# Optimization experiments

Hardware: AMD Instinct MI355X
Metric: run time of the kernel (lower is better)

Reference implementation:

```python
import jax, jax.numpy as jnp
import numpy as np

N_TOKENS = 32768
INPUT_DIM = 1024
HIDDEN_DIM = 256
NUM_EXPERTS = 64
TOP_K = 2


def setup_inputs() -> dict:
    key = jax.random.key(0)
    kx, k1, k2, kb1, kb2 = jax.random.split(key, 5)
    # torch nn.Linear init scale ~ U(-1/sqrt(fan_in), 1/sqrt(fan_in)); use small normals
    x = jax.random.normal(kx, (N_TOKENS, INPUT_DIM), dtype=jnp.float32)
    w1 = jax.random.normal(k1, (HIDDEN_DIM, INPUT_DIM), dtype=jnp.float32) / np.sqrt(INPUT_DIM)
    b1 = jax.random.normal(kb1, (HIDDEN_DIM,), dtype=jnp.float32) * 0.01
    w2 = jax.random.normal(k2, (NUM_EXPERTS, HIDDEN_DIM), dtype=jnp.float32) / np.sqrt(HIDDEN_DIM)
    b2 = jax.random.normal(kb2, (NUM_EXPERTS,), dtype=jnp.float32) * 0.01
    return {"x": x, "w1": w1, "b1": b1, "w2": w2, "b2": b2}


def reference(x, w1, b1, w2, b2):
    # logits = Linear -> ReLU -> Linear
    h = jax.nn.relu(jnp.einsum("nd,hd->nh", x, w1) + b1)       # [N, hidden]
    logits = jnp.einsum("nh,eh->ne", h, w2) + b2               # [N, experts]
    top_k_logits, top_k_indices = jax.lax.top_k(logits, TOP_K)  # [N, k]
    top_k_gates = jax.nn.softmax(top_k_logits, axis=-1)
    return top_k_indices, top_k_gates
```

## Files before the change

### kernel.cpp

```cpp
#include <hip/hip_runtime.h>
#include <math.h>

#define N_TOK 32768
#define IN_DIM 1024
#define HID 256
#define NE 64

__global__ __launch_bounds__(256, 2)
void gemm1_relu(const float* __restrict__ x, const float* __restrict__ w1,
                const float* __restrict__ b1, float* __restrict__ h)
{
    __shared__ float Xs[32][72];
    __shared__ float Ws[32][256];

    const int tid = threadIdx.x;
    const int t0  = blockIdx.x * 64;
    const int tg  = tid >> 5;
    const int hg  = tid & 31;

    float acc[8][8];
    #pragma unroll
    for (int i = 0; i < 8; ++i)
        #pragma unroll
        for (int j = 0; j < 8; ++j) acc[i][j] = 0.f;

    for (int k0 = 0; k0 < IN_DIM; k0 += 32) {
        #pragma unroll
        for (int r = 0; r < 2; ++r) {
            int slot = tid + 256 * r;
            int t  = slot >> 3;
            int kq = (slot & 7) * 4;
            float4 v = *(const float4*)(x + (size_t)(t0 + t) * IN_DIM + k0 + kq);
            Xs[kq + 0][t] = v.x; Xs[kq + 1][t] = v.y;
            Xs[kq + 2][t] = v.z; Xs[kq + 3][t] = v.w;
        }
        #pragma unroll
        for (int r = 0; r < 8; ++r) {
            int slot = tid + 256 * r;
            int hh = slot >> 3;
            int kq = (slot & 7) * 4;
            float4 v = *(const float4*)(w1 + (size_t)hh * IN_DIM + k0 + kq);
            Ws[kq + 0][hh] = v.x; Ws[kq + 1][hh] = v.y;
            Ws[kq + 2][hh] = v.z; Ws[kq + 3][hh] = v.w;
        }
        __syncthreads();

        #pragma unroll
        for (int k = 0; k < 32; ++k) {
            float xv[8], wv[8];
            *(float4*)&xv[0] = *(const float4*)&Xs[k][tg * 8];
            *(float4*)&xv[4] = *(const float4*)&Xs[k][tg * 8 + 4];
            *(float4*)&wv[0] = *(const float4*)&Ws[k][hg * 8];
            *(float4*)&wv[4] = *(const float4*)&Ws[k][hg * 8 + 4];
            #pragma unroll
            for (int i = 0; i < 8; ++i)
                #pragma unroll
                for (int j = 0; j < 8; ++j)
                    acc[i][j] = fmaf(xv[i], wv[j], acc[i][j]);
        }
        __syncthreads();
    }

    float4 bv0 = *(const float4*)(b1 + hg * 8);
    float4 bv1 = *(const float4*)(b1 + hg * 8 + 4);
    float bias[8] = {bv0.x, bv0.y, bv0.z, bv0.w, bv1.x, bv1.y, bv1.z, bv1.w};
    #pragma unroll
    for (int i = 0; i < 8; ++i) {
        int t = t0 + tg * 8 + i;
        float4 o0, o1;
        o0.x = fmaxf(acc[i][0] + bias[0], 0.f);
        o0.y = fmaxf(acc[i][1] + bias[1], 0.f);
        o0.z = fmaxf(acc[i][2] + bias[2], 0.f);
        o0.w = fmaxf(acc[i][3] + bias[3], 0.f);
        o1.x = fmaxf(acc[i][4] + bias[4], 0.f);
        o1.y = fmaxf(acc[i][5] + bias[5], 0.f);
        o1.z = fmaxf(acc[i][6] + bias[6], 0.f);
        o1.w = fmaxf(acc[i][7] + bias[7], 0.f);
        *(float4*)(h + (size_t)t * HID + hg * 8)     = o0;
        *(float4*)(h + (size_t)t * HID + hg * 8 + 4) = o1;
    }
}

__global__ __launch_bounds__(256, 2)
void gemm2_topk(const float* __restrict__ h, const float* __restrict__ w2,
                const float* __restrict__ b2, float* __restrict__ out)
{
    __shared__ float Hs[32][72];
    __shared__ float W2s[32][64];
    __shared__ float Ls[64][65];

    const int tid = threadIdx.x;
    const int t0  = blockIdx.x * 64;
    const int tg  = tid >> 4;
    const int eg  = tid & 15;

    float acc[4][4];
    #pragma unroll
    for (int i = 0; i < 4; ++i)
        #pragma unroll
        for (int j = 0; j < 4; ++j) acc[i][j] = 0.f;

    for (int k0 = 0; k0 < HID; k0 += 32) {
        #pragma unroll
        for (int r = 0; r < 2; ++r) {
            int slot = tid + 256 * r;
            int t  = slot >> 3;
            int kq = (slot & 7) * 4;
            float4 v = *(const float4*)(h + (size_t)(t0 + t) * HID + k0 + kq);
            Hs[kq + 0][t] = v.x; Hs[kq + 1][t] = v.y;
            Hs[kq + 2][t] = v.z; Hs[kq + 3][t] = v.w;
        }
        #pragma unroll
        for (int r = 0; r < 2; ++r) {
            int slot = tid + 256 * r;
            int e  = slot >> 3;
            int kq = (slot & 7) * 4;
            float4 v = *(const float4*)(w2 + (size_t)e * HID + k0 + kq);
            W2s[kq + 0][e] = v.x; W2s[kq + 1][e] = v.y;
            W2s[kq + 2][e] = v.z; W2s[kq + 3][e] = v.w;
        }
        __syncthreads();

        #pragma unroll
        for (int k = 0; k < 32; ++k) {
            float hv[4], wv[4];
            *(float4*)&hv[0] = *(const float4*)&Hs[k][tg * 4];
            *(float4*)&wv[0] = *(const float4*)&W2s[k][eg * 4];
            #pragma unroll
            for (int i = 0; i < 4; ++i)
                #pragma unroll
                for (int j = 0; j < 4; ++j)
                    acc[i][j] = fmaf(hv[i], wv[j], acc[i][j]);
        }
        __syncthreads();
    }

    float4 b2v = *(const float4*)(b2 + eg * 4);
    float bb[4] = {b2v.x, b2v.y, b2v.z, b2v.w};
    #pragma unroll
    for (int i = 0; i < 4; ++i)
        #pragma unroll
        for (int j = 0; j < 4; ++j)
            Ls[tg * 4 + i][eg * 4 + j] = acc[i][j] + bb[j];
    __syncthreads();

    if (tid < 64) {
        const int t = tid;
        float m1 = -INFINITY, m2 = -INFINITY;
        int i1 = 0, i2 = 0;
        #pragma unroll 8
        for (int e = 0; e < NE; ++e) {
            float v = Ls[t][e];
            if (v > m1) { m2 = m1; i2 = i1; m1 = v; i1 = e; }
            else if (v > m2) { m2 = v; i2 = e; }
        }
        float e2  = expf(m2 - m1);
        float inv = 1.f / (1.f + e2);
        float g1  = inv;
        float g2  = e2 * inv;
        int gt = t0 + t;
        out[(size_t)gt * 2 + 0] = (float)i1;
        out[(size_t)gt * 2 + 1] = (float)i2;
        out[(size_t)2 * N_TOK + (size_t)gt * 2 + 0] = g1;
        out[(size_t)2 * N_TOK + (size_t)gt * 2 + 1] = g2;
    }
}

extern "C" void kernel_launch(void* const* d_in, const int* in_sizes, int n_in,
                              void* d_out, int out_size, void* d_ws, size_t ws_size,
                              hipStream_t stream) {
    const float* x  = (const float*)d_in[0];
    const float* w1 = (const float*)d_in[1];
    const float* b1 = (const float*)d_in[2];
    const float* w2 = (const float*)d_in[3];
    const float* b2 = (const float*)d_in[4];
    float* out = (float*)d_out;
    float* h   = (float*)d_ws;

    gemm1_relu<<<N_TOK / 64, 256, 0, stream>>>(x, w1, b1, h);
    gemm2_topk<<<N_TOK / 64, 256, 0, stream>>>(h, w2, b2, out);
}
```

Before: 416.5 us.

## Register-prefetch next K tile, remap wave tiling and pad shared arrays

```diff
diff --git a/kernel.cpp b/kernel.cpp
--- a/kernel.cpp
+++ b/kernel.cpp
@@ -6,17 +6,28 @@
 #define HID 256
 #define NE 64
 
+#define PX 68
+#define PW 260
+#define PL 65
+
 __global__ __launch_bounds__(256, 2)
 void gemm1_relu(const float* __restrict__ x, const float* __restrict__ w1,
                 const float* __restrict__ b1, float* __restrict__ h)
 {
-    __shared__ float Xs[32][72];
-    __shared__ float Ws[32][256];
-
-    const int tid = threadIdx.x;
-    const int t0  = blockIdx.x * 64;
-    const int tg  = tid >> 5;
-    const int hg  = tid & 31;
+    __shared__ float Xs[32 * PX];
+    __shared__ float Ws[32 * PW];
+
+    const int tid  = threadIdx.x;
+    const int t0   = blockIdx.x * 64;
+    const int wave = tid >> 6;
+    const int lane = tid & 63;
+    const int tg   = lane >> 3;
+    const int hg   = lane & 7;
+    const int xoff = tg * 8;
+    const int woff = wave * 64 + hg * 8;
+
+    const int tx = tid >> 3;
+    const int kq = (tid & 7) * 4;
 
     float acc[8][8];
     #pragma unroll
@@ -24,49 +35,65 @@
         #pragma unroll
         for (int j = 0; j < 8; ++j) acc[i][j] = 0.f;
 
-    for (int k0 = 0; k0 < IN_DIM; k0 += 32) {
-        #pragma unroll
-        for (int r = 0; r < 2; ++r) {
-            int slot = tid + 256 * r;
-            int t  = slot >> 3;
-            int kq = (slot & 7) * 4;
-            float4 v = *(const float4*)(x + (size_t)(t0 + t) * IN_DIM + k0 + kq);
-            Xs[kq + 0][t] = v.x; Xs[kq + 1][t] = v.y;
-            Xs[kq + 2][t] = v.z; Xs[kq + 3][t] = v.w;
-        }
-        #pragma unroll
-        for (int r = 0; r < 8; ++r) {
-            int slot = tid + 256 * r;
-            int hh = slot >> 3;
-            int kq = (slot & 7) * 4;
-            float4 v = *(const float4*)(w1 + (size_t)hh * IN_DIM + k0 + kq);
-            Ws[kq + 0][hh] = v.x; Ws[kq + 1][hh] = v.y;
-            Ws[kq + 2][hh] = v.z; Ws[kq + 3][hh] = v.w;
-        }
-        __syncthreads();
+    float4 xr0, xr1, wr[8];
+    {
+        xr0 = *(const float4*)(x + (size_t)(t0 + tx) * IN_DIM + kq);
+        xr1 = *(const float4*)(x + (size_t)(t0 + tx + 32) * IN_DIM + kq);
+        #pragma unroll
+        for (int r = 0; r < 8; ++r)
+            wr[r] = *(const float4*)(w1 + (size_t)(tx + 32 * r) * IN_DIM + kq);
+    }
+
+    for (int kt = 0; kt < 32; ++kt) {
+        __syncthreads();
+        {
+            const float* xp0 = (const float*)&xr0;
+            const float* xp1 = (const float*)&xr1;
+            #pragma unroll
+            for (int j = 0; j < 4; ++j) {
+                Xs[(kq + j) * PX + tx]      = xp0[j];
+                Xs[(kq + j) * PX + tx + 32] = xp1[j];
+            }
+            #pragma unroll
+            for (int r = 0; r < 8; ++r) {
+                const float* wp = (const float*)&wr[r];
+                #pragma unroll
+                for (int j = 0; j < 4; ++j)
+                    Ws[(kq + j) * PW + tx + 32 * r] = wp[j];
+            }
+        }
+        __syncthreads();
+
+        if (kt < 31) {
+            const int k0 = (kt + 1) * 32;
+            xr0 = *(const float4*)(x + (size_t)(t0 + tx) * IN_DIM + k0 + kq);
+            xr1 = *(const float4*)(x + (size_t)(t0 + tx + 32) * IN_DIM + k0 + kq);
+            #pragma unroll
+            for (int r = 0; r < 8; ++r)
+                wr[r] = *(const float4*)(w1 + (size_t)(tx + 32 * r) * IN_DIM + k0 + kq);
+        }
 
         #pragma unroll
         for (int k = 0; k < 32; ++k) {
             float xv[8], wv[8];
-            *(float4*)&xv[0] = *(const float4*)&Xs[k][tg * 8];
-            *(float4*)&xv[4] = *(const float4*)&Xs[k][tg * 8 + 4];
-            *(float4*)&wv[0] = *(const float4*)&Ws[k][hg * 8];
-            *(float4*)&wv[4] = *(const float4*)&Ws[k][hg * 8 + 4];
+            *(float4*)&xv[0] = *(const float4*)&Xs[k * PX + xoff];
+            *(float4*)&xv[4] = *(const float4*)&Xs[k * PX + xoff + 4];
+            *(float4*)&wv[0] = *(const float4*)&Ws[k * PW + woff];
+            *(float4*)&wv[4] = *(const float4*)&Ws[k * PW + woff + 4];
             #pragma unroll
             for (int i = 0; i < 8; ++i)
                 #pragma unroll
                 for (int j = 0; j < 8; ++j)
                     acc[i][j] = fmaf(xv[i], wv[j], acc[i][j]);
         }
-        __syncthreads();
-    }
-
-    float4 bv0 = *(const float4*)(b1 + hg * 8);
-    float4 bv1 = *(const float4*)(b1 + hg * 8 + 4);
-    float bias[8] = {bv0.x, bv0.y, bv0.z, bv0.w, bv1.x, bv1.y, bv1.z, bv1.w};
+    }
+
+    float bias[8];
+    *(float4*)&bias[0] = *(const float4*)(b1 + woff);
+    *(float4*)&bias[4] = *(const float4*)(b1 + woff + 4);
     #pragma unroll
     for (int i = 0; i < 8; ++i) {
-        int t = t0 + tg * 8 + i;
+        const int t = t0 + xoff + i;
         float4 o0, o1;
         o0.x = fmaxf(acc[i][0] + bias[0], 0.f);
         o0.y = fmaxf(acc[i][1] + bias[1], 0.f);
@@ -76,8 +103,8 @@
         o1.y = fmaxf(acc[i][5] + bias[5], 0.f);
         o1.z = fmaxf(acc[i][6] + bias[6], 0.f);
         o1.w = fmaxf(acc[i][7] + bias[7], 0.f);
-        *(float4*)(h + (size_t)t * HID + hg * 8)     = o0;
-        *(float4*)(h + (size_t)t * HID + hg * 8 + 4) = o1;
+        *(float4*)(h + (size_t)t * HID + woff)     = o0;
+        *(float4*)(h + (size_t)t * HID + woff + 4) = o1;
     }
 }
 
@@ -85,14 +112,21 @@
 void gemm2_topk(const float* __restrict__ h, const float* __restrict__ w2,
                 const float* __restrict__ b2, float* __restrict__ out)
 {
-    __shared__ float Hs[32][72];
-    __shared__ float W2s[32][64];
-    __shared__ float Ls[64][65];
-
-    const int tid = threadIdx.x;
-    const int t0  = blockIdx.x * 64;
-    const int tg  = tid >> 4;
-    const int eg  = tid & 15;
+    __shared__ float Hs[32 * PX];
+    __shared__ float W2s[32 * PX];
+    __shared__ float Ls[64 * PL];
+
+    const int tid  = threadIdx.x;
+    const int t0   = blockIdx.x * 64;
+    const int wave = tid >> 6;
+    const int lane = tid & 63;
+    const int tg4  = lane >> 2;
+    const int eg   = lane & 3;
+    const int toff = tg4 * 4;
+    const int eoff = wave * 16 + eg * 4;
+
+    const int tx = tid >> 3;
+    const int kq = (tid & 7) * 4;
 
     float acc[4][4];
     #pragma unroll
@@ -100,48 +134,57 @@
         #pragma unroll
         for (int j = 0; j < 4; ++j) acc[i][j] = 0.f;
 
-    for (int k0 = 0; k0 < HID; k0 += 32) {
-        #pragma unroll
-        for (int r = 0; r < 2; ++r) {
-            int slot = tid + 256 * r;
-            int t  = slot >> 3;
-            int kq = (slot & 7) * 4;
-            float4 v = *(const float4*)(h + (size_t)(t0 + t) * HID + k0 + kq);
-            Hs[kq + 0][t] = v.x; Hs[kq + 1][t] = v.y;
-            Hs[kq + 2][t] = v.z; Hs[kq + 3][t] = v.w;
-        }
-        #pragma unroll
-        for (int r = 0; r < 2; ++r) {
-            int slot = tid + 256 * r;
-            int e  = slot >> 3;
-            int kq = (slot & 7) * 4;
-            float4 v = *(const float4*)(w2 + (size_t)e * HID + k0 + kq);
-            W2s[kq + 0][e] = v.x; W2s[kq + 1][e] = v.y;
-            W2s[kq + 2][e] = v.z; W2s[kq + 3][e] = v.w;
-        }
-        __syncthreads();
+    float4 hr0, hr1, wr0, wr1;
+    hr0 = *(const float4*)(h + (size_t)(t0 + tx) * HID + kq);
+    hr1 = *(const float4*)(h + (size_t)(t0 + tx + 32) * HID + kq);
+    wr0 = *(const float4*)(w2 + (size_t)tx * HID + kq);
+    wr1 = *(const float4*)(w2 + (size_t)(tx + 32) * HID + kq);
+
+    for (int kt = 0; kt < 8; ++kt) {
+        __syncthreads();
+        {
+            const float* p0 = (const float*)&hr0;
+            const float* p1 = (const float*)&hr1;
+            const float* q0 = (const float*)&wr0;
+            const float* q1 = (const float*)&wr1;
+            #pragma unroll
+            for (int j = 0; j < 4; ++j) {
+                Hs[(kq + j) * PX + tx]       = p0[j];
+                Hs[(kq + j) * PX + tx + 32]  = p1[j];
+                W2s[(kq + j) * PX + tx]      = q0[j];
+                W2s[(kq + j) * PX + tx + 32] = q1[j];
+            }
+        }
+        __syncthreads();
+
+        if (kt < 7) {
+            const int k0 = (kt + 1) * 32;
+            hr0 = *(const float4*)(h + (size_t)(t0 + tx) * HID + k0 + kq);
+            hr1 = *(const float4*)(h + (size_t)(t0 + tx + 32) * HID + k0 + kq);
+            wr0 = *(const float4*)(w2 + (size_t)tx * HID + k0 + kq);
+            wr1 = *(const float4*)(w2 + (size_t)(tx + 32) * HID + k0 + kq);
+        }
 
         #pragma unroll
         for (int k = 0; k < 32; ++k) {
             float hv[4], wv[4];
-            *(float4*)&hv[0] = *(const float4*)&Hs[k][tg * 4];
-            *(float4*)&wv[0] = *(const float4*)&W2s[k][eg * 4];
+            *(float4*)&hv[0] = *(const float4*)&Hs[k * PX + toff];
+            *(float4*)&wv[0] = *(const float4*)&W2s[k * PX + eoff];
             #pragma unroll
             for (int i = 0; i < 4; ++i)
                 #pragma unroll
                 for (int j = 0; j < 4; ++j)
                     acc[i][j] = fmaf(hv[i], wv[j], acc[i][j]);
         }
-        __syncthreads();
-    }
-
-    float4 b2v = *(const float4*)(b2 + eg * 4);
-    float bb[4] = {b2v.x, b2v.y, b2v.z, b2v.w};
+    }
+
+    float bb[4];
+    *(float4*)&bb[0] = *(const float4*)(b2 + eoff);
     #pragma unroll
     for (int i = 0; i < 4; ++i)
         #pragma unroll
         for (int j = 0; j < 4; ++j)
-            Ls[tg * 4 + i][eg * 4 + j] = acc[i][j] + bb[j];
+            Ls[(toff + i) * PL + eoff + j] = acc[i][j] + bb[j];
     __syncthreads();
 
     if (tid < 64) {
@@ -150,19 +193,17 @@
         int i1 = 0, i2 = 0;
         #pragma unroll 8
         for (int e = 0; e < NE; ++e) {
-            float v = Ls[t][e];
+            float v = Ls[t * PL + e];
             if (v > m1) { m2 = m1; i2 = i1; m1 = v; i1 = e; }
             else if (v > m2) { m2 = v; i2 = e; }
         }
         float e2  = expf(m2 - m1);
         float inv = 1.f / (1.f + e2);
-        float g1  = inv;
-        float g2  = e2 * inv;
-        int gt = t0 + t;
+        const int gt = t0 + t;
         out[(size_t)gt * 2 + 0] = (float)i1;
         out[(size_t)gt * 2 + 1] = (float)i2;
-        out[(size_t)2 * N_TOK + (size_t)gt * 2 + 0] = g1;
-        out[(size_t)2 * N_TOK + (size_t)gt * 2 + 1] = g2;
+        out[(size_t)2 * N_TOK + (size_t)gt * 2 + 0] = inv;
+        out[(size_t)2 * N_TOK + (size_t)gt * 2 + 1] = e2 * inv;
     }
 }
 
```

Result: slower. 511.5 us (+22.8%).

## Replace LDS-tiled GEMMs with per-wave register GEMMs over pre-transposed weights

Applied to the files above, without the earlier changes.

```diff
diff --git a/kernel.cpp b/kernel.cpp
--- a/kernel.cpp
+++ b/kernel.cpp
@@ -5,164 +5,169 @@
 #define IN_DIM 1024
 #define HID 256
 #define NE 64
+#define MT 8
+#define KU 4
 
-__global__ __launch_bounds__(256, 2)
-void gemm1_relu(const float* __restrict__ x, const float* __restrict__ w1,
+
+__global__ void prep_transpose(const float* __restrict__ w1, const float* __restrict__ w2,
+                               float* __restrict__ w1t, float* __restrict__ w2t)
+{
+    __shared__ float t[32][33];
+    const int b = blockIdx.x;
+    const float* src; float* dst; int R, C, bx, by;
+    if (b < 256) { src = w1; dst = w1t; R = HID; C = IN_DIM; bx = (b & 31) * 32; by = (b >> 5) * 32; }
+    else { int bb = b - 256; src = w2; dst = w2t; R = NE; C = HID; bx = (bb & 7) * 32; by = (bb >> 3) * 32; }
+    const int lx = threadIdx.x & 31, ly = threadIdx.x >> 5;
+    #pragma unroll
+    for (int j = 0; j < 4; ++j)
+        t[ly + 8 * j][lx] = src[(size_t)(by + ly + 8 * j) * C + bx + lx];
+    __syncthreads();
+    #pragma unroll
+    for (int j = 0; j < 4; ++j)
+        dst[(size_t)(bx + ly + 8 * j) * R + by + lx] = t[lx][ly + 8 * j];
+}
+
+__global__ __launch_bounds__(256)
+void gemm1_relu(const float* __restrict__ x, const float* __restrict__ w1t,
                 const float* __restrict__ b1, float* __restrict__ h)
 {
-    __shared__ float Xs[32][72];
-    __shared__ float Ws[32][256];
+    const int lane = threadIdx.x & 63;
+    const int wv   = __builtin_amdgcn_readfirstlane(threadIdx.x >> 6);
+    const int tb   = blockIdx.x * (4 * MT) + wv * MT;
+    const float* xb = x + (size_t)tb * IN_DIM;
+    const float* wb = w1t + lane * 4;
 
-    const int tid = threadIdx.x;
-    const int t0  = blockIdx.x * 64;
-    const int tg  = tid >> 5;
-    const int hg  = tid & 31;
+    float acc[MT][4];
+    #pragma unroll
+    for (int i = 0; i < MT; ++i)
+        #pragma unroll
+        for (int j = 0; j < 4; ++j) acc[i][j] = 0.f;
 
-    float acc[8][8];
+    float4 xA[MT], xB[MT], wA[KU], wB[KU];
     #pragma unroll
-    for (int i = 0; i < 8; ++i)
+    for (int i = 0; i < MT; ++i) xA[i] = *(const float4*)(xb + i * IN_DIM);
+    #pragma unroll
+    for (int u = 0; u < KU; ++u) wA[u] = *(const float4*)(wb + u * HID);
+
+    for (int k0 = 0; k0 < IN_DIM; k0 += 2 * KU) {
+        const int kb = k0 + KU;
         #pragma unroll
-        for (int j = 0; j < 8; ++j) acc[i][j] = 0.f;
-
-    for (int k0 = 0; k0 < IN_DIM; k0 += 32) {
+        for (int i = 0; i < MT; ++i) xB[i] = *(const float4*)(xb + i * IN_DIM + kb);
         #pragma unroll
-        for (int r = 0; r < 2; ++r) {
-            int slot = tid + 256 * r;
-            int t  = slot >> 3;
-            int kq = (slot & 7) * 4;
-            float4 v = *(const float4*)(x + (size_t)(t0 + t) * IN_DIM + k0 + kq);
-            Xs[kq + 0][t] = v.x; Xs[kq + 1][t] = v.y;
-            Xs[kq + 2][t] = v.z; Xs[kq + 3][t] = v.w;
-        }
-        #pragma unroll
-        for (int r = 0; r < 8; ++r) {
-            int slot = tid + 256 * r;
-            int hh = slot >> 3;
-            int kq = (slot & 7) * 4;
-            float4 v = *(const float4*)(w1 + (size_t)hh * IN_DIM + k0 + kq);
-            Ws[kq + 0][hh] = v.x; Ws[kq + 1][hh] = v.y;
-            Ws[kq + 2][hh] = v.z; Ws[kq + 3][hh] = v.w;
-        }
-        __syncthreads();
+        for (int u = 0; u < KU; ++u) wB[u] = *(const float4*)(wb + (size_t)(kb + u) * HID);
 
         #pragma unroll
-        for (int k = 0; k < 32; ++k) {
-            float xv[8], wv[8];
-            *(float4*)&xv[0] = *(const float4*)&Xs[k][tg * 8];
-            *(float4*)&xv[4] = *(const float4*)&Xs[k][tg * 8 + 4];
-            *(float4*)&wv[0] = *(const float4*)&Ws[k][hg * 8];
-            *(float4*)&wv[4] = *(const float4*)&Ws[k][hg * 8 + 4];
+        for (int u = 0; u < KU; ++u)
             #pragma unroll
-            for (int i = 0; i < 8; ++i)
-                #pragma unroll
-                for (int j = 0; j < 8; ++j)
-                    acc[i][j] = fmaf(xv[i], wv[j], acc[i][j]);
-        }
-        __syncthreads();
+            for (int i = 0; i < MT; ++i) {
+                const float xs = ((const float*)&xA[i])[u];
+                acc[i][0] = fmaf(xs, wA[u].x, acc[i][0]);
+                acc[i][1] = fmaf(xs, wA[u].y, acc[i][1]);
+                acc[i][2] = fmaf(xs, wA[u].z, acc[i][2]);
+                acc[i][3] = fmaf(xs, wA[u].w, acc[i][3]);
+            }
+
+        int ka = k0 + 2 * KU; ka = (ka < IN_DIM) ? ka : 0;
+        #pragma unroll
+        for (int i = 0; i < MT; ++i) xA[i] = *(const float4*)(xb + i * IN_DIM + ka);
+        #pragma unroll
+        for (int u = 0; u < KU; ++u) wA[u] = *(const float4*)(wb + (size_t)(ka + u) * HID);
+
+        #pragma unroll
+        for (int u = 0; u < KU; ++u)
+            #pragma unroll
+            for (int i = 0; i < MT; ++i) {
+                const float xs = ((const float*)&xB[i])[u];
+                acc[i][0] = fmaf(xs, wB[u].x, acc[i][0]);
+                acc[i][1] = fmaf(xs, wB[u].y, acc[i][1]);
+                acc[i][2] = fmaf(xs, wB[u].z, acc[i][2]);
+                acc[i][3] = fmaf(xs, wB[u].w, acc[i][3]);
+            }
     }
 
-    float4 bv0 = *(const float4*)(b1 + hg * 8);
-    float4 bv1 = *(const float4*)(b1 + hg * 8 + 4);
-    float bias[8] = {bv0.x, bv0.y, bv0.z, bv0.w, bv1.x, bv1.y, bv1.z, bv1.w};
+    const float4 bv = *(const float4*)(b1 + lane * 4);
     #pragma unroll
-    for (int i = 0; i < 8; ++i) {
-        int t = t0 + tg * 8 + i;
-        float4 o0, o1;
-        o0.x = fmaxf(acc[i][0] + bias[0], 0.f);
-        o0.y = fmaxf(acc[i][1] + bias[1], 0.f);
-        o0.z = fmaxf(acc[i][2] + bias[2], 0.f);
-        o0.w = fmaxf(acc[i][3] + bias[3], 0.f);
-        o1.x = fmaxf(acc[i][4] + bias[4], 0.f);
-        o1.y = fmaxf(acc[i][5] + bias[5], 0.f);
-        o1.z = fmaxf(acc[i][6] + bias[6], 0.f);
-        o1.w = fmaxf(acc[i][7] + bias[7], 0.f);
-        *(float4*)(h + (size_t)t * HID + hg * 8)     = o0;
-        *(float4*)(h + (size_t)t * HID + hg * 8 + 4) = o1;
+    for (int i = 0; i < MT; ++i) {
+        float4 o;
+        o.x = fmaxf(acc[i][0] + bv.x, 0.f);
+        o.y = fmaxf(acc[i][1] + bv.y, 0.f);
+        o.z = fmaxf(acc[i][2] + bv.z, 0.f);
+        o.w = fmaxf(acc[i][3] + bv.w, 0.f);
+        *(float4*)(h + (size_t)(tb + i) * HID + lane * 4) = o;
     }
 }
 
-__global__ __launch_bounds__(256, 2)
-void gemm2_topk(const float* __restrict__ h, const float* __restrict__ w2,
+__global__ __launch_bounds__(256)
+void gemm2_topk(const float* __restrict__ h, const float* __restrict__ w2t,
                 const float* __restrict__ b2, float* __restrict__ out)
 {
-    __shared__ float Hs[32][72];
-    __shared__ float W2s[32][64];
-    __shared__ float Ls[64][65];
+    __shared__ float Ls[4][MT][NE + 1];
 
-    const int tid = threadIdx.x;
-    const int t0  = blockIdx.x * 64;
-    const int tg  = tid >> 4;
-    const int eg  = tid & 15;
+    const int lane = threadIdx.x & 63;
+    const int wv   = __builtin_amdgcn_readfirstlane(threadIdx.x >> 6);
+    const int tb   = blockIdx.x * (4 * MT) + wv * MT;
+    const float* hb = h + (size_t)tb * HID;
+    const float* wb = w2t + lane;
 
-    float acc[4][4];
+    float acc[MT];
     #pragma unroll
-    for (int i = 0; i < 4; ++i)
+    for (int i = 0; i < MT; ++i) acc[i] = 0.f;
+
+    float4 xA[MT], xB[MT];
+    float  wA[KU], wB[KU];
+    #pragma unroll
+    for (int i = 0; i < MT; ++i) xA[i] = *(const float4*)(hb + i * HID);
+    #pragma unroll
+    for (int u = 0; u < KU; ++u) wA[u] = wb[(size_t)u * NE];
+
+    for (int k0 = 0; k0 < HID; k0 += 2 * KU) {
+        const int kb = k0 + KU;
         #pragma unroll
-        for (int j = 0; j < 4; ++j) acc[i][j] = 0.f;
-
-    for (int k0 = 0; k0 < HID; k0 += 32) {
+        for (int i = 0; i < MT; ++i) xB[i] = *(const float4*)(hb + i * HID + kb);
         #pragma unroll
-        for (int r = 0; r < 2; ++r) {
-            int slot = tid + 256 * r;
-            int t  = slot >> 3;
-            int kq = (slot & 7) * 4;
-            float4 v = *(const float4*)(h + (size_t)(t0 + t) * HID + k0 + kq);
-            Hs[kq + 0][t] = v.x; Hs[kq + 1][t] = v.y;
-            Hs[kq + 2][t] = v.z; Hs[kq + 3][t] = v.w;
-        }
-        #pragma unroll
-        for (int r = 0; r < 2; ++r) {
-            int slot = tid + 256 * r;
-            int e  = slot >> 3;
-            int kq = (slot & 7) * 4;
-            float4 v = *(const float4*)(w2 + (size_t)e * HID + k0 + kq);
-            W2s[kq + 0][e] = v.x; W2s[kq + 1][e] = v.y;
-            W2s[kq + 2][e] = v.z; W2s[kq + 3][e] = v.w;
-        }
-        __syncthreads();
+        for (int u = 0; u < KU; ++u) wB[u] = wb[(size_t)(kb + u) * NE];
 
         #pragma unroll
-        for (int k = 0; k < 32; ++k) {
-            float hv[4], wv[4];
-            *(float4*)&hv[0] = *(const float4*)&Hs[k][tg * 4];
-            *(float4*)&wv[0] = *(const float4*)&W2s[k][eg * 4];
+        for (int u = 0; u < KU; ++u)
             #pragma unroll
-            for (int i = 0; i < 4; ++i)
-                #pragma unroll
-                for (int j = 0; j < 4; ++j)
-                    acc[i][j] = fmaf(hv[i], wv[j], acc[i][j]);
-        }
-        __syncthreads();
+            for (int i = 0; i < MT; ++i)
+                acc[i] = fmaf(((const float*)&xA[i])[u], wA[u], acc[i]);
+
+        int ka = k0 + 2 * KU; ka = (ka < HID) ? ka : 0;
+        #pragma unroll
+        for (int i = 0; i < MT; ++i) xA[i] = *(const float4*)(hb + i * HID + ka);
+        #pragma unroll
+        for (int u = 0; u < KU; ++u) wA[u] = wb[(size_t)(ka + u) * NE];
+
+        #pragma unroll
+        for (int u = 0; u < KU; ++u)
+            #pragma unroll
+            for (int i = 0; i < MT; ++i)
+                acc[i] = fmaf(((const float*)&xB[i])[u], wB[u], acc[i]);
     }
 
-    float4 b2v = *(const float4*)(b2 + eg * 4);
-    float bb[4] = {b2v.x, b2v.y, b2v.z, b2v.w};
+    const float bb = b2[lane];
     #pragma unroll
-    for (int i = 0; i < 4; ++i)
-        #pragma unroll
-        for (int j = 0; j < 4; ++j)
-            Ls[tg * 4 + i][eg * 4 + j] = acc[i][j] + bb[j];
-    __syncthreads();
+    for (int i = 0; i < MT; ++i)
+        Ls[wv][i][lane] = acc[i] + bb;
 
-    if (tid < 64) {
-        const int t = tid;
+    if (lane < MT) {
+        const int t = lane;
         float m1 = -INFINITY, m2 = -INFINITY;
         int i1 = 0, i2 = 0;
         #pragma unroll 8
         for (int e = 0; e < NE; ++e) {
-            float v = Ls[t][e];
+            float v = Ls[wv][t][e];
             if (v > m1) { m2 = m1; i2 = i1; m1 = v; i1 = e; }
             else if (v > m2) { m2 = v; i2 = e; }
         }
         float e2  = expf(m2 - m1);
         float inv = 1.f / (1.f + e2);
-        float g1  = inv;
-        float g2  = e2 * inv;
-        int gt = t0 + t;
+        const int gt = tb + t;
         out[(size_t)gt * 2 + 0] = (float)i1;
         out[(size_t)gt * 2 + 1] = (float)i2;
-        out[(size_t)2 * N_TOK + (size_t)gt * 2 + 0] = g1;
-        out[(size_t)2 * N_TOK + (size_t)gt * 2 + 1] = g2;
+        out[(size_t)2 * N_TOK + (size_t)gt * 2 + 0] = inv;
+        out[(size_t)2 * N_TOK + (size_t)gt * 2 + 1] = e2 * inv;
     }
 }
 
@@ -175,8 +180,12 @@
     const float* w2 = (const float*)d_in[3];
     const float* b2 = (const float*)d_in[4];
     float* out = (float*)d_out;
-    float* h   = (float*)d_ws;
 
-    gemm1_relu<<<N_TOK / 64, 256, 0, stream>>>(x, w1, b1, h);
-    gemm2_topk<<<N_TOK / 64, 256, 0, stream>>>(h, w2, b2, out);
+    float* w1t = (float*)d_ws;
+    float* w2t = w1t + (size_t)IN_DIM * HID;
+    float* h   = w2t + (size_t)HID * NE;
+
+    prep_transpose<<<272, 256, 0, stream>>>(w1, w2, w1t, w2t);
+    gemm1_relu<<<N_TOK / (4 * MT), 256, 0, stream>>>(x, w1t, b1, h);
+    gemm2_topk<<<N_TOK / (4 * MT), 256, 0, stream>>>(h, w2t, b2, out);
 }
```

Result: slower. 472.0 us (+13.3%).
